# Performance work log

Measured on AMD Instinct MI355X. Metric: run time of the kernel, lower is better.

Reference implementation:

```python
import jax, jax.numpy as jnp
import numpy as np

D_MODEL = 2048
N_HEADS = 32
N_KV = 8
HEAD_DIM = D_MODEL // N_HEADS  # 64
D_FF = 8192
ROPE_BASE = 10000.0
EPS = 1e-5
B, S = 2, 2048


def setup_inputs() -> dict:
    key = jax.random.key(0)
    ks = jax.random.split(key, 8)
    s = 0.02
    qkv_out = (N_HEADS + 2 * N_KV) * HEAD_DIM
    return {
        "x": jax.random.normal(ks[0], (B, S, D_MODEL), jnp.float32),
        "w_norm1": jnp.ones((D_MODEL,), jnp.float32),
        "w_qkv": jax.random.normal(ks[1], (D_MODEL, qkv_out), jnp.float32) * s,
        "w_out": jax.random.normal(ks[2], (D_MODEL, D_MODEL), jnp.float32) * s,
        "w_norm2": jnp.ones((D_MODEL,), jnp.float32),
        "w_gate": jax.random.normal(ks[3], (D_MODEL, D_FF), jnp.float32) * s,
        "w_up": jax.random.normal(ks[4], (D_MODEL, D_FF), jnp.float32) * s,
        "w_down": jax.random.normal(ks[5], (D_FF, D_MODEL), jnp.float32) * s,
    }


def _rmsnorm(x, w):
    var = jnp.mean(x * x, axis=-1, keepdims=True)
    return x * jax.lax.rsqrt(var + EPS) * w


def _rope(x, cos, sin):
    # x: [b, s, h, d]; cos/sin: [s, d/2]; non-interleaved (NeoX half split)
    half = x.shape[-1] // 2
    x1, x2 = x[..., :half], x[..., half:]
    c = cos[None, :, None, :]
    sn = sin[None, :, None, :]
    return jnp.concatenate([x1 * c - x2 * sn, x1 * sn + x2 * c], axis=-1)


def _forward(x, w_norm1, w_qkv, w_out, w_norm2, w_gate, w_up, w_down):
    b, s, d = x.shape
    # --- attention block ---
    h = _rmsnorm(x, w_norm1)
    qkv = h @ w_qkv  # [b, s, (H + 2*KV) * hd]
    q = qkv[..., : N_HEADS * HEAD_DIM].reshape(b, s, N_HEADS, HEAD_DIM)
    kv = qkv[..., N_HEADS * HEAD_DIM:].reshape(b, s, 2, N_KV, HEAD_DIM)
    k, v = kv[:, :, 0], kv[:, :, 1]

    inv_freq = 1.0 / (ROPE_BASE ** (jnp.arange(0, HEAD_DIM, 2, dtype=jnp.float32) / HEAD_DIM))
    t = jnp.arange(s, dtype=jnp.float32)
    freqs = t[:, None] * inv_freq[None, :]  # [s, hd/2]
    cos, sin = jnp.cos(freqs), jnp.sin(freqs)
    q = _rope(q, cos, sin)
    k = _rope(k, cos, sin)

    # GQA: repeat_interleave kv heads to match q heads
    g = N_HEADS // N_KV
    k = jnp.repeat(k, g, axis=2)  # [b, s, H, hd]
    v = jnp.repeat(v, g, axis=2)

    scale = 1.0 / np.sqrt(HEAD_DIM)
    scores = jnp.einsum("bqhd,bkhd->bhqk", q, k) * scale
    causal = jnp.tril(jnp.ones((s, s), bool))
    scores = jnp.where(causal[None, None], scores, jnp.finfo(scores.dtype).min)
    attn = jax.nn.softmax(scores, axis=-1)
    ctx = jnp.einsum("bhqk,bkhd->bqhd", attn, v).reshape(b, s, N_HEADS * HEAD_DIM)
    x = x + ctx @ w_out

    # --- MLP block (SwiGLU) ---
    h2 = _rmsnorm(x, w_norm2)
    mlp = (jax.nn.silu(h2 @ w_gate) * (h2 @ w_up)) @ w_down
    return x + mlp


def reference(x, w_norm1, w_qkv, w_out, w_norm2, w_gate, w_up, w_down):
    return _forward(x, w_norm1, w_qkv, w_out, w_norm2, w_gate, w_up, w_down)
```

## Files before the change

kernel.cpp:

```cpp
#include <hip/hip_runtime.h>
#include <stdint.h>

#define D_MODEL 2048
#define S_LEN   2048
#define NTOK    4096
#define QKV_N   3072
#define DFF     8192

typedef float  f32x4   __attribute__((ext_vector_type(4)));
typedef float  f32x16  __attribute__((ext_vector_type(16)));
typedef __bf16 bf16x8  __attribute__((ext_vector_type(8)));
typedef unsigned short u16;
typedef unsigned short u16x8 __attribute__((ext_vector_type(8)));

__device__ __forceinline__ float b2f(u16 u){ union{float f; uint32_t i;} v; v.i = ((uint32_t)u) << 16; return v.f; }
__device__ __forceinline__ u16 f2b(float f){
  union{float f; uint32_t i;} v; v.f = f;
  uint32_t r = v.i + 0x7FFFu + ((v.i >> 16) & 1u);
  return (u16)(r >> 16);
}

__device__ __forceinline__ void gload_lds16(const void* gsrc, void* ldst){
  __builtin_amdgcn_global_load_lds(
      (const __attribute__((address_space(1))) void*)gsrc,
      (__attribute__((address_space(3))) void*)ldst,
      16, 0, 0);
}

__device__ __forceinline__ void conv_tiles(const float* W, u16* WT,
    int Nfull, int Kt, int Nt, int k0g, int n0g, void* ldsbuf)
{
  if (W == nullptr) return;
  float* tf = (float*)ldsbuf;
  const int tt  = threadIdx.x;
  const int nTn = Nt >> 6;
  const int nT  = (Kt >> 6) * nTn;
  const int bid = blockIdx.y * gridDim.x + blockIdx.x;
  const int gsz = gridDim.x * gridDim.y;
  const int c4 = (tt & 15) << 2;
  const int r  = tt >> 4;
  for (int tile = bid; tile < nT; tile += gsz) {
    const int k0 = (tile / nTn) << 6, n0 = (tile % nTn) << 6;
    __syncthreads();
    if (tt < 256) {
#pragma unroll
      for (int i = 0; i < 4; ++i) {
        int row = r + i * 16;
        float4 v = *reinterpret_cast<const float4*>(&W[(size_t)(k0g + k0 + row) * Nfull + n0g + n0 + c4]);
        tf[row * 65 + c4 + 0] = v.x; tf[row * 65 + c4 + 1] = v.y;
        tf[row * 65 + c4 + 2] = v.z; tf[row * 65 + c4 + 3] = v.w;
      }
    }
    __syncthreads();
    if (tt < 256) {
#pragma unroll
      for (int i = 0; i < 4; ++i) {
        int n = r + i * 16;
        ushort4 ov;
        ov.x = f2b(tf[(c4 + 0) * 65 + n]); ov.y = f2b(tf[(c4 + 1) * 65 + n]);
        ov.z = f2b(tf[(c4 + 2) * 65 + n]); ov.w = f2b(tf[(c4 + 3) * 65 + n]);
        *reinterpret_cast<ushort4*>(&WT[(size_t)(n0 + n) * Kt + k0 + c4]) = ov;
      }
    }
  }
}

__global__ __launch_bounds__(256) void wconv_kernel(const float* __restrict__ W, u16* __restrict__ WT,
                                                    int Nfull, int Kt, int Nt, int k0g, int n0g)
{
  __shared__ float tile[64 * 65];
  conv_tiles(W, WT, Nfull, Kt, Nt, k0g, n0g, tile);
}

__global__ void sincos_kernel(float* __restrict__ ct, float* __restrict__ st)
{
  int idx = blockIdx.x * 256 + threadIdx.x;
  if (idx >= S_LEN * 32) return;
  int p = idx >> 5, i = idx & 31;
  double freq = pow(10000.0, -((double)(2*i)) / 64.0);
  double ang  = (double)p * freq;
  ct[idx] = (float)cos(ang);
  st[idx] = (float)sin(ang);
}

template<bool BF16IN>
__global__ __launch_bounds__(256) void rmsnorm_kernel(const void* __restrict__ xin, const float* __restrict__ w, u16* __restrict__ out,
                                                      const float* cvW, u16* cvWT, int cvNfull, int cvKt, int cvNt, int cvK0g, int cvN0g)
{
  __shared__ float tfbuf[64 * 65];
  const int row = blockIdx.x;
  const int t = threadIdx.x;
  float v[8];
  if (BF16IN) {
    const u16* xr = ((const u16*)xin) + (size_t)row * D_MODEL;
    u16x8 a = *reinterpret_cast<const u16x8*>(&xr[t*8]);
#pragma unroll
    for (int j = 0; j < 8; ++j) v[j] = b2f(a[j]);
  } else {
    const float* xr = ((const float*)xin) + (size_t)row * D_MODEL;
    float4 a = *reinterpret_cast<const float4*>(&xr[t*8]);
    float4 c = *reinterpret_cast<const float4*>(&xr[t*8+4]);
    v[0]=a.x; v[1]=a.y; v[2]=a.z; v[3]=a.w; v[4]=c.x; v[5]=c.y; v[6]=c.z; v[7]=c.w;
  }
  float ss = 0.f;
#pragma unroll
  for (int j = 0; j < 8; ++j) ss += v[j]*v[j];
#pragma unroll
  for (int d = 1; d < 64; d <<= 1) ss += __shfl_xor(ss, d);
  __shared__ float red[4];
  if ((t & 63) == 0) red[t >> 6] = ss;
  __syncthreads();
  ss = red[0] + red[1] + red[2] + red[3];
  const float sc = rsqrtf(ss * (1.0f / (float)D_MODEL) + 1e-5f);
  float4 w0 = *reinterpret_cast<const float4*>(&w[t*8]);
  float4 w1 = *reinterpret_cast<const float4*>(&w[t*8+4]);
  u16x8 o;
  o[0]=f2b(v[0]*sc*w0.x); o[1]=f2b(v[1]*sc*w0.y); o[2]=f2b(v[2]*sc*w0.z); o[3]=f2b(v[3]*sc*w0.w);
  o[4]=f2b(v[4]*sc*w1.x); o[5]=f2b(v[5]*sc*w1.y); o[6]=f2b(v[6]*sc*w1.z); o[7]=f2b(v[7]*sc*w1.w);
  *reinterpret_cast<u16x8*>(&out[(size_t)row * D_MODEL + t*8]) = o;
  conv_tiles(cvW, cvWT, cvNfull, cvKt, cvNt, cvK0g, cvN0g, tfbuf);
}

template<int EPI>
__device__ __forceinline__ void epi_store(size_t idx, float v, float* Cf, u16* Cb,
                                          const float* resf, const u16* resb, const u16* other)
{
  if (EPI == 2)      Cb[idx] = f2b(v / (1.0f + __expf(-v)));
  else if (EPI == 3) Cb[idx] = f2b(v * b2f(other[idx]));
  else if (EPI == 4) Cb[idx] = f2b(v);
  else if (EPI == 5) Cf[idx] += v;
  else if (EPI == 6) Cb[idx] = f2b(v + resf[idx]);
  else if (EPI == 7) Cf[idx] = v + b2f(resb[idx]);
}

template<int EPI>
__global__ __launch_bounds__(512, 2) void gemm8p_kernel(
    const u16* __restrict__ A, const u16* __restrict__ BT,
    int K, int lda, int ldb, int ldc, int n_off,
    float* Cf, u16* Cb,
    const float* __restrict__ resf, const u16* __restrict__ resb, const u16* other,
    const float* cvW, u16* cvWT, int cvNfull, int cvKt, int cvNt, int cvK0g, int cvN0g)
{
  __shared__ u16 lds[65536];
  const int tid = threadIdx.x;
  const int w = tid >> 6, lane = tid & 63;
  const int g = lane >> 4, lr = lane & 15;
  const int wm = w >> 2, wn = w & 3;
  const int bn = blockIdx.x, bm = blockIdx.y;
  const int NT = K >> 6;
  const int NI = NT >> 1;

  const int srow = tid >> 3;
  const int sg   = (tid & 7) ^ (srow & 7);
  const u16* Asrc = A  + (size_t)(bm * 256) * lda;
  const u16* Bsrc = BT + (size_t)(bn * 256) * ldb;

  const int agc0 = ((0 + g) ^ (lr & 7)) * 8;
  const int agc1 = ((4 + g) ^ (lr & 7)) * 8;

  f32x4 acc[8][4];
#pragma unroll
  for (int i = 0; i < 8; ++i)
#pragma unroll
    for (int j = 0; j < 4; ++j) acc[i][j] = (f32x4){0.f, 0.f, 0.f, 0.f};
  bf16x8 af[4][2], bf0[2][2], bf1[2][2];

#define STAGE_H(isB, h, b, T) do {                                           \
    int tc = ((T) < NT) ? (T) : (NT - 1);                                    \
    const u16* sb = (isB) ? Bsrc : Asrc;                                     \
    const int  sld = (isB) ? ldb : lda;                                      \
    const u16* s0 = sb + (size_t)((h)*128 + srow) * sld + tc*64 + sg*8;      \
    u16* dst = &lds[(b)*32768 + (isB)*16384 + (h)*8192 + tid*8];             \
    gload_lds16(s0, dst);                                                    \
    gload_lds16(s0 + (size_t)64 * sld, dst + 4096);                          \
  } while (0)

#define LOADA(mih, b) { _Pragma("unroll") for (int q = 0; q < 4; ++q) {      \
    const u16* rp = &lds[(b)*32768 + (wm*128 + (mih)*64 + q*16 + lr) * 64];  \
    af[q][0] = *(const bf16x8*)(rp + agc0);                                  \
    af[q][1] = *(const bf16x8*)(rp + agc1); } }

#define LOADB(dst, nih, b) { _Pragma("unroll") for (int nq = 0; nq < 2; ++nq) { \
    const u16* rp = &lds[(b)*32768 + 16384 + (wn*64 + (nih)*32 + nq*16 + lr) * 64]; \
    dst[nq][0] = *(const bf16x8*)(rp + agc0);                                \
    dst[nq][1] = *(const bf16x8*)(rp + agc1); } }

#define MM(mih, nih, BF) {                                                   \
    __builtin_amdgcn_s_setprio(1);                                           \
    _Pragma("unroll") for (int kk = 0; kk < 2; ++kk)                         \
      _Pragma("unroll") for (int q = 0; q < 4; ++q)                          \
        _Pragma("unroll") for (int nq = 0; nq < 2; ++nq)                     \
          acc[(mih)*4+q][(nih)*2+nq] = __builtin_amdgcn_mfma_f32_16x16x32_bf16( \
              af[q][kk], BF[nq][kk], acc[(mih)*4+q][(nih)*2+nq], 0, 0, 0);   \
    __builtin_amdgcn_s_setprio(0); }

#define SYNC_MID  __builtin_amdgcn_s_barrier();                              \
                  asm volatile("s_waitcnt lgkmcnt(0)" ::: "memory");         \
                  __builtin_amdgcn_sched_barrier(0);
#define PHEND     __builtin_amdgcn_s_barrier();
#define PHEND_VM  asm volatile("s_waitcnt vmcnt(4)" ::: "memory");           \
                  __builtin_amdgcn_s_barrier();

  STAGE_H(0, 0, 0, 0); STAGE_H(0, 1, 0, 0);
  STAGE_H(1, 0, 0, 0); STAGE_H(1, 1, 0, 0);
  STAGE_H(1, 0, 1, 1); STAGE_H(1, 1, 1, 1);
  asm volatile("s_waitcnt vmcnt(4)" ::: "memory");
  __builtin_amdgcn_s_barrier();

  for (int i = 0; i < NI; ++i) {
    const int t0 = 2 * i;
    LOADA(0, 0); LOADB(bf0, 0, 0);
    STAGE_H(0, 0, 1, t0 + 1);
    SYNC_MID; MM(0, 0, bf0); PHEND;
    LOADB(bf1, 1, 0);
    STAGE_H(0, 1, 1, t0 + 1);
    SYNC_MID; MM(0, 1, bf1); PHEND;
    LOADA(1, 0);
    STAGE_H(1, 0, 0, t0 + 2);
    SYNC_MID; MM(1, 1, bf1); PHEND;
    STAGE_H(1, 1, 0, t0 + 2);
    SYNC_MID; MM(1, 0, bf0); PHEND_VM;
    LOADA(0, 1); LOADB(bf0, 0, 1);
    STAGE_H(0, 0, 0, t0 + 2);
    SYNC_MID; MM(0, 0, bf0); PHEND;
    LOADB(bf1, 1, 1);
    STAGE_H(0, 1, 0, t0 + 2);
    SYNC_MID; MM(0, 1, bf1); PHEND;
    LOADA(1, 1);
    STAGE_H(1, 0, 1, t0 + 3);
    SYNC_MID; MM(1, 1, bf1); PHEND;
    STAGE_H(1, 1, 1, t0 + 3);
    SYNC_MID; MM(1, 0, bf0); PHEND_VM;
  }
#undef STAGE_H
#undef LOADA
#undef LOADB
#undef MM

#pragma unroll
  for (int mi = 0; mi < 8; ++mi) {
    const int rowOff = (mi >> 2) * 64 + (mi & 3) * 16;
#pragma unroll
    for (int ni = 0; ni < 4; ++ni) {
      const int colOff = (ni >> 1) * 32 + (ni & 1) * 16;
#pragma unroll
      for (int j = 0; j < 4; ++j) {
        int row = bm*256 + wm*128 + rowOff + g*4 + j;
        int col = n_off + bn*256 + wn*64 + colOff + lr;
        epi_store<EPI>((size_t)row * ldc + col, acc[mi][ni][j], Cf, Cb, resf, resb, other);
      }
    }
  }
  conv_tiles(cvW, cvWT, cvNfull, cvKt, cvNt, cvK0g, cvN0g, lds);
}

template<int EPI>
__global__ __launch_bounds__(512) void gemm128_kernel(
    const u16* __restrict__ A, const u16* __restrict__ BT,
    int K, int lda, int ldb, int ldc, int n_off,
    float* Cf, u16* Cb,
    const float* __restrict__ resf, const u16* __restrict__ resb, const u16* other,
    const float* cvW, u16* cvWT, int cvNfull, int cvKt, int cvNt, int cvK0g, int cvN0g)
{
  __shared__ u16 lds[49152];
  const int tid = threadIdx.x;
  const int w = tid >> 6, lane = tid & 63;
  const int g = lane >> 4, lr = lane & 15;
  const int wm = w >> 2, wn = w & 3;
  const int bn = blockIdx.x, bm = blockIdx.y;
  const int NT = K >> 6;
  const int NI = NT >> 1;

  const int srow = tid >> 3;
  const int sg   = (tid & 7) ^ (srow & 7);
  const u16* Asrc = A  + (size_t)(bm * 128) * lda;
  const u16* Bsrc = BT + (size_t)(bn * 256) * ldb;

  const int agc0 = ((0 + g) ^ (lr & 7)) * 8;
  const int agc1 = ((4 + g) ^ (lr & 7)) * 8;

  f32x4 acc[4][4];
#pragma unroll
  for (int i = 0; i < 4; ++i)
#pragma unroll
    for (int j = 0; j < 4; ++j) acc[i][j] = (f32x4){0.f, 0.f, 0.f, 0.f};
  bf16x8 af[2][2], bf0[2][2], bf1[2][2];

#define STAGE_A(b, T) do {                                                   \
    int tc = ((T) < NT) ? (T) : (NT - 1);                                    \
    const u16* s0 = Asrc + (size_t)srow * lda + tc*64 + sg*8;                \
    u16* dst = &lds[(b)*24576 + tid*8];                                      \
    gload_lds16(s0, dst);                                                    \
    gload_lds16(s0 + (size_t)64 * lda, dst + 4096);                          \
  } while (0)

#define STAGE_BH(h, b, T) do {                                               \
    int tc = ((T) < NT) ? (T) : (NT - 1);                                    \
    const u16* s0 = Bsrc + (size_t)((h)*128 + srow) * ldb + tc*64 + sg*8;    \
    u16* dst = &lds[(b)*24576 + 8192 + (h)*8192 + tid*8];                    \
    gload_lds16(s0, dst);                                                    \
    gload_lds16(s0 + (size_t)64 * ldb, dst + 4096);                         \
  } while (0)

#define LOADA(mih, b) { _Pragma("unroll") for (int q = 0; q < 2; ++q) {      \
    const u16* rp = &lds[(b)*24576 + (wm*64 + (mih)*32 + q*16 + lr) * 64];   \
    af[q][0] = *(const bf16x8*)(rp + agc0);                                  \
    af[q][1] = *(const bf16x8*)(rp + agc1); } }

#define LOADB(dst, nih, b) { _Pragma("unroll") for (int nq = 0; nq < 2; ++nq) { \
    const u16* rp = &lds[(b)*24576 + 8192 + (wn*64 + (nih)*32 + nq*16 + lr) * 64]; \
    dst[nq][0] = *(const bf16x8*)(rp + agc0);                                \
    dst[nq][1] = *(const bf16x8*)(rp + agc1); } }

#define MM(mih, nih, BF) {                                                   \
    __builtin_amdgcn_s_setprio(1);                                           \
    _Pragma("unroll") for (int kk = 0; kk < 2; ++kk)                         \
      _Pragma("unroll") for (int q = 0; q < 2; ++q)                          \
        _Pragma("unroll") for (int nq = 0; nq < 2; ++nq)                     \
          acc[(mih)*2+q][(nih)*2+nq] = __builtin_amdgcn_mfma_f32_16x16x32_bf16( \
              af[q][kk], BF[nq][kk], acc[(mih)*2+q][(nih)*2+nq], 0, 0, 0);   \
    __builtin_amdgcn_s_setprio(0); }

  STAGE_A(0, 0); STAGE_BH(0, 0, 0); STAGE_BH(1, 0, 0);
  STAGE_BH(0, 1, 1); STAGE_BH(1, 1, 1);
  asm volatile("s_waitcnt vmcnt(4)" ::: "memory");
  __builtin_amdgcn_s_barrier();

  for (int i = 0; i < NI; ++i) {
    const int t0 = 2 * i;
    LOADA(0, 0); LOADB(bf0, 0, 0);
    STAGE_A(1, t0 + 1);
    SYNC_MID; MM(0, 0, bf0); PHEND;
    LOADB(bf1, 1, 0);
    STAGE_BH(0, 0, t0 + 2);
    SYNC_MID; MM(0, 1, bf1); PHEND;
    LOADA(1, 0);
    STAGE_BH(1, 0, t0 + 2);
    SYNC_MID; MM(1, 1, bf1); PHEND;
    STAGE_A(0, t0 + 2);
    SYNC_MID; MM(1, 0, bf0);
    asm volatile("s_waitcnt vmcnt(6)" ::: "memory");
    __builtin_amdgcn_s_barrier();
    LOADA(0, 1); LOADB(bf0, 0, 1);
    SYNC_MID; MM(0, 0, bf0); PHEND;
    LOADB(bf1, 1, 1);
    STAGE_BH(0, 1, t0 + 3);
    SYNC_MID; MM(0, 1, bf1); PHEND;
    LOADA(1, 1);
    STAGE_BH(1, 1, t0 + 3);
    SYNC_MID; MM(1, 1, bf1); PHEND;
    SYNC_MID; MM(1, 0, bf0);
    asm volatile("s_waitcnt vmcnt(4)" ::: "memory");
    __builtin_amdgcn_s_barrier();
  }
#undef STAGE_A
#undef STAGE_BH
#undef LOADA
#undef LOADB
#undef MM
#undef SYNC_MID
#undef PHEND
#undef PHEND_VM

#pragma unroll
  for (int mi = 0; mi < 4; ++mi) {
    const int rowOff = (mi >> 1) * 32 + (mi & 1) * 16;
#pragma unroll
    for (int ni = 0; ni < 4; ++ni) {
      const int colOff = (ni >> 1) * 32 + (ni & 1) * 16;
#pragma unroll
      for (int j = 0; j < 4; ++j) {
        int row = bm*128 + wm*64 + rowOff + g*4 + j;
        int col = n_off + bn*256 + wn*64 + colOff + lr;
        epi_store<EPI>((size_t)row * ldc + col, acc[mi][ni][j], Cf, Cb, resf, resb, other);
      }
    }
  }
  conv_tiles(cvW, cvWT, cvNfull, cvKt, cvNt, cvK0g, cvN0g, lds);
}

__global__ __launch_bounds__(256) void rope_kernel(
    const u16* __restrict__ qkv, const float* __restrict__ ct, const float* __restrict__ st,
    u16* __restrict__ Kt, u16* __restrict__ VT)
{
  const int tok = blockIdx.x;
  const int b = tok >> 11, s = tok & (S_LEN - 1);
  const int w = threadIdx.x >> 6, lane = threadIdx.x & 63;
  const size_t base = (size_t)tok * QKV_N;
  for (int slot = w; slot < 16; slot += 4) {
    int col = (slot < 8) ? 2048 + slot * 64 : 2560 + (slot - 8) * 64;
    float v = b2f(qkv[base + col + lane]);
    if (slot < 8) {
      int i = lane & 31;
      float c = ct[s * 32 + i], sn = st[s * 32 + i];
      float p = b2f(qkv[base + col + (lane ^ 32)]);
      v = (lane < 32) ? (v * c - p * sn) : (v * c + p * sn);
    }
    u16 ob = f2b(v);
    if (slot < 8) Kt[((size_t)(b * 8 + slot)     * S_LEN + s) * 64 + lane] = ob;
    else          VT[((size_t)(b * 8 + slot - 8) * 64 + lane) * S_LEN + s] = ob;
  }
}

#define ASCALE 0.1803368801111204f
__global__ __launch_bounds__(256, 3) void attn_kernel(
    const u16* __restrict__ qkv, const u16* __restrict__ Kt,
    const u16* __restrict__ VT, u16* __restrict__ ctx,
    const float* __restrict__ ct, const float* __restrict__ st,
    const float* cvW, u16* cvWT, int cvNfull, int cvKt, int cvNt, int cvK0g, int cvN0g)
{
  __shared__ float tfbuf[64 * 65];
  const int bh  = blockIdx.x;
  const int qb  = 15 - blockIdx.y;
  const int wid = threadIdx.x >> 6;
  const int lane = threadIdx.x & 63;
  const int b = bh >> 5, h = bh & 31;
  const int kvh = (b << 3) + (h >> 2);
  const int q0 = qb * 128 + wid * 32;
  const int cq = lane & 31;
  const int hi = lane >> 5;

  const u16* Kp = Kt + (size_t)kvh * S_LEN * 64 + cq * 64 + hi * 8;
  const u16* Vbase = VT + (size_t)kvh * 64 * S_LEN + hi * 8;
  const u16* Vp[4];
#pragma unroll
  for (int v = 0; v < 4; ++v)
    Vp[v] = Vbase + (size_t)((v & 1) * 32 + cq) * S_LEN + (v >> 1) * 16;

  bf16x8 qf[4];
  {
    const u16* Qr = qkv + (size_t)(b * S_LEN + q0 + cq) * QKV_N + h * 64 + hi * 8;
    u16 qr[4][8];
#pragma unroll
    for (int t = 0; t < 4; ++t)
      *reinterpret_cast<u16x8*>(qr[t]) = *reinterpret_cast<const u16x8*>(Qr + t * 16);
    const float* cb = ct + (size_t)(q0 + cq) * 32 + hi * 8;
    const float* sb = st + (size_t)(q0 + cq) * 32 + hi * 8;
    union { u16 u[8]; bf16x8 v; } qo[4];
#pragma unroll
    for (int t = 0; t < 2; ++t) {
      float4 c0 = *reinterpret_cast<const float4*>(cb + 16 * t);
      float4 c1 = *reinterpret_cast<const float4*>(cb + 16 * t + 4);
      float4 s0 = *reinterpret_cast<const float4*>(sb + 16 * t);
      float4 s1 = *reinterpret_cast<const float4*>(sb + 16 * t + 4);
      float cc[8] = {c0.x,c0.y,c0.z,c0.w, c1.x,c1.y,c1.z,c1.w};
      float ssn[8] = {s0.x,s0.y,s0.z,s0.w, s1.x,s1.y,s1.z,s1.w};
#pragma unroll
      for (int i = 0; i < 8; ++i) {
        float lo = b2f(qr[t][i]), hif = b2f(qr[t + 2][i]);
        qo[t].u[i]     = f2b(lo * cc[i] - hif * ssn[i]);
        qo[t + 2].u[i] = f2b(hif * cc[i] + lo * ssn[i]);
      }
    }
#pragma unroll
    for (int t = 0; t < 4; ++t) qf[t] = qo[t].v;
  }

  f32x16 o0 = {}, o1 = {};
  float m = -1e30f, l = 0.f;

  __shared__ float xch[4][32];

  const int nt = qb * 4 + wid + 1;

#define ATT_LOADK(KF, T) { _Pragma("unroll") for (int q_ = 0; q_ < 4; ++q_) \
    KF[q_] = *(const bf16x8*)(Kp + (T) * 2048 + q_ * 16); }
#define ATT_LOADV(VF, T) { _Pragma("unroll") for (int v_ = 0; v_ < 4; ++v_) \
    VF[v_] = *(const bf16x8*)(Vp[v_] + (T) * 32); }

#define ATT_COMPUTE(KF, VF, T) do {                                          \
    f32x16 sA = {}, sB = {};                                                 \
    sA = __builtin_amdgcn_mfma_f32_32x32x16_bf16(KF[0], qf[0], sA, 0, 0, 0); \
    sB = __builtin_amdgcn_mfma_f32_32x32x16_bf16(KF[1], qf[1], sB, 0, 0, 0); \
    sA = __builtin_amdgcn_mfma_f32_32x32x16_bf16(KF[2], qf[2], sA, 0, 0, 0); \
    sB = __builtin_amdgcn_mfma_f32_32x32x16_bf16(KF[3], qf[3], sB, 0, 0, 0); \
    float p[16];                                                             \
    _Pragma("unroll") for (int r = 0; r < 16; ++r) p[r] = (sA[r] + sB[r]) * ASCALE; \
    if ((T) == nt - 1) {                                                     \
      _Pragma("unroll") for (int r = 0; r < 16; ++r) {                       \
        int kk = (r & 3) + 8 * (r >> 2) + 4 * hi;                            \
        if (kk > cq) p[r] = -1e30f;                                          \
      }                                                                      \
    }                                                                        \
    float m0_ = fmaxf(fmaxf(p[0], p[1]), p[2]);                              \
    float m1_ = fmaxf(fmaxf(p[3], p[4]), p[5]);                              \
    float m2_ = fmaxf(fmaxf(p[6], p[7]), p[8]);                              \
    float m3_ = fmaxf(fmaxf(p[9], p[10]), p[11]);                            \
    float m4_ = fmaxf(fmaxf(p[12], p[13]), p[14]);                           \
    float tmax = fmaxf(fmaxf(fmaxf(m0_, m1_), m2_), fmaxf(fmaxf(m3_, m4_), p[15])); \
    tmax = fmaxf(tmax, __shfl_xor(tmax, 32));                                \
    if (!__all(tmax <= m + 8.0f)) {                                          \
      float mn = fmaxf(m, tmax);                                             \
      float corr = exp2f(m - mn);                                            \
      m = mn;                                                                \
      l *= corr;                                                             \
      if (hi == 0) xch[wid][cq] = corr;                                      \
      asm volatile("s_waitcnt lgkmcnt(0)" ::: "memory");                     \
      __builtin_amdgcn_sched_barrier(0);                                     \
      float4 c0 = *reinterpret_cast<const float4*>(&xch[wid][4 * hi + 0]);   \
      float4 c1 = *reinterpret_cast<const float4*>(&xch[wid][4 * hi + 8]);   \
      float4 c2 = *reinterpret_cast<const float4*>(&xch[wid][4 * hi + 16]);  \
      float4 c3 = *reinterpret_cast<const float4*>(&xch[wid][4 * hi + 24]);  \
      float ca[16] = {c0.x,c0.y,c0.z,c0.w, c1.x,c1.y,c1.z,c1.w,              \
                      c2.x,c2.y,c2.z,c2.w, c3.x,c3.y,c3.z,c3.w};             \
      _Pragma("unroll") for (int r = 0; r < 16; ++r) { o0[r] *= ca[r]; o1[r] *= ca[r]; } \
    }                                                                        \
    float tsum = 0.f;                                                        \
    _Pragma("unroll") for (int r = 0; r < 16; ++r) { p[r] = exp2f(p[r] - m); tsum += p[r]; } \
    l += tsum;                                                               \
    uint32_t wds[8], pw[8];                                                  \
    _Pragma("unroll") for (int j = 0; j < 8; ++j) {                          \
      uint32_t wv;                                                           \
      asm("v_cvt_pk_bf16_f32 %0, %1, %2" : "=v"(wv) : "v"(p[2*j]), "v"(p[2*j+1])); \
      wds[j] = wv;                                                           \
    }                                                                        \
    _Pragma("unroll") for (int j = 0; j < 8; ++j) pw[j] = __shfl_xor(wds[j], 32); \
    union { uint32_t u[4]; bf16x8 v; } pa0, pa1;                             \
    pa0.u[0] = hi ? pw[2]  : wds[0];                                         \
    pa0.u[1] = hi ? pw[3]  : wds[1];                                         \
    pa0.u[2] = hi ? wds[2] : pw[0];                                          \
    pa0.u[3] = hi ? wds[3] : pw[1];                                          \
    pa1.u[0] = hi ? pw[6]  : wds[4];                                         \
    pa1.u[1] = hi ? pw[7]  : wds[5];                                         \
    pa1.u[2] = hi ? wds[6] : pw[4];                                          \
    pa1.u[3] = hi ? wds[7] : pw[5];                                          \
    o0 = __builtin_amdgcn_mfma_f32_32x32x16_bf16(pa0.v, VF[0], o0, 0, 0, 0); \
    o0 = __builtin_amdgcn_mfma_f32_32x32x16_bf16(pa1.v, VF[2], o0, 0, 0, 0); \
    o1 = __builtin_amdgcn_mfma_f32_32x32x16_bf16(pa0.v, VF[1], o1, 0, 0, 0); \
    o1 = __builtin_amdgcn_mfma_f32_32x32x16_bf16(pa1.v, VF[3], o1, 0, 0, 0); \
  } while (0)

  bf16x8 kf0[4], kf1[4], vf[4];
  ATT_LOADK(kf0, 0);
  for (int t = 0; t < nt; ) {
    if (t + 1 < nt) ATT_LOADK(kf1, t + 1);
    ATT_LOADV(vf, t);
    ATT_COMPUTE(kf0, vf, t);
    ++t; if (t >= nt) break;
    if (t + 1 < nt) ATT_LOADK(kf0, t + 1);
    ATT_LOADV(vf, t);
    ATT_COMPUTE(kf1, vf, t);
    ++t;
  }
#undef ATT_LOADK
#undef ATT_LOADV
#undef ATT_COMPUTE

  l += __shfl_xor(l, 32);
  float linv = 1.0f / l;
  if (hi == 0) xch[wid][cq] = linv;
  asm volatile("s_waitcnt lgkmcnt(0)" ::: "memory");
  __builtin_amdgcn_sched_barrier(0);
  float4 n0 = *reinterpret_cast<const float4*>(&xch[wid][4 * hi + 0]);
  float4 n1 = *reinterpret_cast<const float4*>(&xch[wid][4 * hi + 8]);
  float4 n2 = *reinterpret_cast<const float4*>(&xch[wid][4 * hi + 16]);
  float4 n3 = *reinterpret_cast<const float4*>(&xch[wid][4 * hi + 24]);
  float na[16] = {n0.x,n0.y,n0.z,n0.w, n1.x,n1.y,n1.z,n1.w,
                  n2.x,n2.y,n2.z,n2.w, n3.x,n3.y,n3.z,n3.w};
#pragma unroll
  for (int r = 0; r < 16; ++r) {
    int row = (r & 3) + 8 * (r >> 2) + 4 * hi;
    size_t base = (size_t)(b * S_LEN + q0 + row) * D_MODEL + h * 64;
    ctx[base + cq]      = f2b(o0[r] * na[r]);
    ctx[base + 32 + cq] = f2b(o1[r] * na[r]);
  }
  conv_tiles(cvW, cvWT, cvNfull, cvKt, cvNt, cvK0g, cvN0g, tfbuf);
}

#define NOCV nullptr, nullptr, 0, 0, 0, 0, 0
extern "C" void kernel_launch(void* const* d_in, const int* in_sizes, int n_in,
                              void* d_out, int out_size, void* d_ws, size_t ws_size,
                              hipStream_t stream)
{
  const float* x     = (const float*)d_in[0];
  const float* wn1   = (const float*)d_in[1];
  const float* wqkv  = (const float*)d_in[2];
  const float* wout  = (const float*)d_in[3];
  const float* wn2   = (const float*)d_in[4];
  const float* wgate = (const float*)d_in[5];
  const float* wup   = (const float*)d_in[6];
  const float* wdown = (const float*)d_in[7];
  float* out = (float*)d_out;
  char* ws = (char*)d_ws;

  float* cosT  = (float*)(ws + 0);
  float* sinT  = (float*)(ws + 262144);
  u16*   slotA = (u16*)  (ws + 524288);
  u16*   slotB = (u16*)  (ws + 17301504);
  u16*   x1b   = (u16*)  (ws + 34078720);
  char*  S     = ws + 50855936;
  u16*   hB    = (u16*)(S + 0);
  u16*   qkvB  = (u16*)(S + 16777216);
  u16*   kB    = (u16*)(S + 41943040);
  u16*   vtB   = (u16*)(S + 46137344);
  u16*   ctxB  = (u16*)(S + 0);
  u16*   h2B   = (u16*)(S + 0);
  u16*   slab  = (u16*)(S + 16777216);

  sincos_kernel<<<dim3(256), 256, 0, stream>>>(cosT, sinT);
  rmsnorm_kernel<false><<<dim3(NTOK), 256, 0, stream>>>(x, wn1, hB, NOCV);
  wconv_kernel<<<dim3(1536), 256, 0, stream>>>(wqkv, slotA, 3072, 2048, 3072, 0, 0);

  gemm128_kernel<4><<<dim3(12, 32), 512, 0, stream>>>(hB, slotA, 2048, 2048, 2048, 3072, 0,
      nullptr, qkvB, nullptr, nullptr, nullptr, wout, slotB, 2048, 2048, 2048, 0, 0);
  rope_kernel<<<dim3(NTOK), 256, 0, stream>>>(qkvB, cosT, sinT, kB, vtB);
  attn_kernel<<<dim3(64, 16), 256, 0, stream>>>(qkvB, kB, vtB, ctxB, cosT, sinT,
      wgate, slotA, 8192, 2048, 4096, 0, 0);

  gemm128_kernel<6><<<dim3(8, 32), 512, 0, stream>>>(ctxB, slotB, 2048, 2048, 2048, 2048, 0,
      nullptr, x1b, x, nullptr, nullptr, NOCV);

  rmsnorm_kernel<true><<<dim3(NTOK), 256, 0, stream>>>(x1b, wn2, h2B,
      wup, slotB, 8192, 2048, 4096, 0, 0);

  gemm8p_kernel<2><<<dim3(16, 16), 512, 0, stream>>>(h2B, slotA, 2048, 2048, 2048, 4096, 0,
      nullptr, slab, nullptr, nullptr, nullptr, NOCV);
  gemm8p_kernel<3><<<dim3(16, 16), 512, 0, stream>>>(h2B, slotB, 2048, 2048, 2048, 4096, 0,
      nullptr, slab, nullptr, nullptr, slab, wdown, slotA, 2048, 4096, 2048, 0, 0);
  gemm128_kernel<7><<<dim3(8, 32), 512, 0, stream>>>(slab, slotA, 4096, 4096, 4096, 2048, 0,
      out, nullptr, nullptr, x1b, nullptr, wgate, slotB, 8192, 2048, 4096, 0, 4096);
  gemm8p_kernel<2><<<dim3(16, 16), 512, 0, stream>>>(h2B, slotB, 2048, 2048, 2048, 4096, 0,
      nullptr, slab, nullptr, nullptr, nullptr, wup, slotA, 8192, 2048, 4096, 0, 4096);
  gemm8p_kernel<3><<<dim3(16, 16), 512, 0, stream>>>(h2B, slotA, 2048, 2048, 2048, 4096, 0,
      nullptr, slab, nullptr, nullptr, slab, wdown, slotB, 2048, 4096, 2048, 4096, 0);
  gemm128_kernel<5><<<dim3(8, 32), 512, 0, stream>>>(slab, slotB, 4096, 4096, 4096, 2048, 0,
      out, nullptr, nullptr, nullptr, nullptr, NOCV);
}
```

Measured before the change: 791.4 us.

## Split-K down projection, rebalance causal attention tasks, fold softmax scale into Q

The down-projection GEMMs now use the 256-tile gemm8p kernel with a split-K grid over blockIdx.z. One K half accumulates into the fp32 output and the other writes bf16 partials, which a new add_partials kernel sums at the end. The residual is copied into out by the second rmsnorm. Attention blocks now each process a pair of complementary causal query tiles (jj and 63-jj) to balance work. They also prefetch V alongside K, fold the softmax scale into Q at load time, use a tree sum for l, and lower launch bounds to 2 waves. Storing partials in bf16 loses precision, and the extra partial buffers and reduction pass add memory traffic.

Result: slower. 854.5 us (+8.0%).

```diff
diff --git a/kernel.cpp b/kernel.cpp
--- a/kernel.cpp
+++ b/kernel.cpp
@@ -35,8 +35,8 @@
   const int tt  = threadIdx.x;
   const int nTn = Nt >> 6;
   const int nT  = (Kt >> 6) * nTn;
-  const int bid = blockIdx.y * gridDim.x + blockIdx.x;
-  const int gsz = gridDim.x * gridDim.y;
+  const int bid = (blockIdx.z * gridDim.y + blockIdx.y) * gridDim.x + blockIdx.x;
+  const int gsz = gridDim.x * gridDim.y * gridDim.z;
   const int c4 = (tt & 15) << 2;
   const int r  = tt >> 4;
   for (int tile = bid; tile < nT; tile += gsz) {
@@ -85,6 +85,7 @@
 
 template<bool BF16IN>
 __global__ __launch_bounds__(256) void rmsnorm_kernel(const void* __restrict__ xin, const float* __restrict__ w, u16* __restrict__ out,
+                                                      float* __restrict__ xout,
                                                       const float* cvW, u16* cvWT, int cvNfull, int cvKt, int cvNt, int cvK0g, int cvN0g)
 {
   __shared__ float tfbuf[64 * 65];
@@ -101,6 +102,12 @@
     float4 a = *reinterpret_cast<const float4*>(&xr[t*8]);
     float4 c = *reinterpret_cast<const float4*>(&xr[t*8+4]);
     v[0]=a.x; v[1]=a.y; v[2]=a.z; v[3]=a.w; v[4]=c.x; v[5]=c.y; v[6]=c.z; v[7]=c.w;
+  }
+  if (xout) {
+    float4 o0 = {v[0], v[1], v[2], v[3]};
+    float4 o1 = {v[4], v[5], v[6], v[7]};
+    *reinterpret_cast<float4*>(&xout[(size_t)row * D_MODEL + t*8])     = o0;
+    *reinterpret_cast<float4*>(&xout[(size_t)row * D_MODEL + t*8 + 4]) = o1;
   }
   float ss = 0.f;
 #pragma unroll
@@ -131,12 +138,13 @@
   else if (EPI == 5) Cf[idx] += v;
   else if (EPI == 6) Cb[idx] = f2b(v + resf[idx]);
   else if (EPI == 7) Cf[idx] = v + b2f(resb[idx]);
+  else if (EPI == 8) { if (blockIdx.z == 0) Cf[idx] += v; else Cb[idx] = f2b(v); }
 }
 
 template<int EPI>
 __global__ __launch_bounds__(512, 2) void gemm8p_kernel(
     const u16* __restrict__ A, const u16* __restrict__ BT,
-    int K, int lda, int ldb, int ldc, int n_off,
+    int K, int lda, int ldb, int ldc, int n_off, int kstep,
     float* Cf, u16* Cb,
     const float* __restrict__ resf, const u16* __restrict__ resb, const u16* other,
     const float* cvW, u16* cvWT, int cvNfull, int cvKt, int cvNt, int cvK0g, int cvN0g)
@@ -147,13 +155,14 @@
   const int g = lane >> 4, lr = lane & 15;
   const int wm = w >> 2, wn = w & 3;
   const int bn = blockIdx.x, bm = blockIdx.y;
+  const int koff = blockIdx.z * kstep;
   const int NT = K >> 6;
   const int NI = NT >> 1;
 
   const int srow = tid >> 3;
   const int sg   = (tid & 7) ^ (srow & 7);
-  const u16* Asrc = A  + (size_t)(bm * 256) * lda;
-  const u16* Bsrc = BT + (size_t)(bn * 256) * ldb;
+  const u16* Asrc = A  + (size_t)(bm * 256) * lda + koff;
+  const u16* Bsrc = BT + (size_t)(bn * 256) * ldb + koff;
 
   const int agc0 = ((0 + g) ^ (lr & 7)) * 8;
   const int agc1 = ((4 + g) ^ (lr & 7)) * 8;
@@ -403,7 +412,7 @@
 }
 
 #define ASCALE 0.1803368801111204f
-__global__ __launch_bounds__(256, 3) void attn_kernel(
+__global__ __launch_bounds__(256, 2) void attn_kernel(
     const u16* __restrict__ qkv, const u16* __restrict__ Kt,
     const u16* __restrict__ VT, u16* __restrict__ ctx,
     const float* __restrict__ ct, const float* __restrict__ st,
@@ -411,12 +420,12 @@
 {
   __shared__ float tfbuf[64 * 65];
   const int bh  = blockIdx.x;
-  const int qb  = 15 - blockIdx.y;
+  const int y   = blockIdx.y;
   const int wid = threadIdx.x >> 6;
   const int lane = threadIdx.x & 63;
   const int b = bh >> 5, h = bh & 31;
   const int kvh = (b << 3) + (h >> 2);
-  const int q0 = qb * 128 + wid * 32;
+  const int jj = y * 4 + wid;
   const int cq = lane & 31;
   const int hi = lane >> 5;
 
@@ -427,41 +436,7 @@
   for (int v = 0; v < 4; ++v)
     Vp[v] = Vbase + (size_t)((v & 1) * 32 + cq) * S_LEN + (v >> 1) * 16;
 
-  bf16x8 qf[4];
-  {
-    const u16* Qr = qkv + (size_t)(b * S_LEN + q0 + cq) * QKV_N + h * 64 + hi * 8;
-    u16 qr[4][8];
-#pragma unroll
-    for (int t = 0; t < 4; ++t)
-      *reinterpret_cast<u16x8*>(qr[t]) = *reinterpret_cast<const u16x8*>(Qr + t * 16);
-    const float* cb = ct + (size_t)(q0 + cq) * 32 + hi * 8;
-    const float* sb = st + (size_t)(q0 + cq) * 32 + hi * 8;
-    union { u16 u[8]; bf16x8 v; } qo[4];
-#pragma unroll
-    for (int t = 0; t < 2; ++t) {
-      float4 c0 = *reinterpret_cast<const float4*>(cb + 16 * t);
-      float4 c1 = *reinterpret_cast<const float4*>(cb + 16 * t + 4);
-      float4 s0 = *reinterpret_cast<const float4*>(sb + 16 * t);
-      float4 s1 = *reinterpret_cast<const float4*>(sb + 16 * t + 4);
-      float cc[8] = {c0.x,c0.y,c0.z,c0.w, c1.x,c1.y,c1.z,c1.w};
-      float ssn[8] = {s0.x,s0.y,s0.z,s0.w, s1.x,s1.y,s1.z,s1.w};
-#pragma unroll
-      for (int i = 0; i < 8; ++i) {
-        float lo = b2f(qr[t][i]), hif = b2f(qr[t + 2][i]);
-        qo[t].u[i]     = f2b(lo * cc[i] - hif * ssn[i]);
-        qo[t + 2].u[i] = f2b(hif * cc[i] + lo * ssn[i]);
-      }
-    }
-#pragma unroll
-    for (int t = 0; t < 4; ++t) qf[t] = qo[t].v;
-  }
-
-  f32x16 o0 = {}, o1 = {};
-  float m = -1e30f, l = 0.f;
-
   __shared__ float xch[4][32];
-
-  const int nt = qb * 4 + wid + 1;
 
 #define ATT_LOADK(KF, T) { _Pragma("unroll") for (int q_ = 0; q_ < 4; ++q_) \
     KF[q_] = *(const bf16x8*)(Kp + (T) * 2048 + q_ * 16); }
@@ -475,7 +450,7 @@
     sA = __builtin_amdgcn_mfma_f32_32x32x16_bf16(KF[2], qf[2], sA, 0, 0, 0); \
     sB = __builtin_amdgcn_mfma_f32_32x32x16_bf16(KF[3], qf[3], sB, 0, 0, 0); \
     float p[16];                                                             \
-    _Pragma("unroll") for (int r = 0; r < 16; ++r) p[r] = (sA[r] + sB[r]) * ASCALE; \
+    _Pragma("unroll") for (int r = 0; r < 16; ++r) p[r] = sA[r] + sB[r];     \
     if ((T) == nt - 1) {                                                     \
       _Pragma("unroll") for (int r = 0; r < 16; ++r) {                       \
         int kk = (r & 3) + 8 * (r >> 2) + 4 * hi;                            \
@@ -505,9 +480,13 @@
                       c2.x,c2.y,c2.z,c2.w, c3.x,c3.y,c3.z,c3.w};             \
       _Pragma("unroll") for (int r = 0; r < 16; ++r) { o0[r] *= ca[r]; o1[r] *= ca[r]; } \
     }                                                                        \
-    float tsum = 0.f;                                                        \
-    _Pragma("unroll") for (int r = 0; r < 16; ++r) { p[r] = exp2f(p[r] - m); tsum += p[r]; } \
-    l += tsum;                                                               \
+    _Pragma("unroll") for (int r = 0; r < 16; ++r) p[r] = exp2f(p[r] - m);   \
+    {                                                                        \
+      float a0 = p[0]+p[1], a1 = p[2]+p[3], a2 = p[4]+p[5], a3 = p[6]+p[7];  \
+      float a4 = p[8]+p[9], a5 = p[10]+p[11], a6 = p[12]+p[13], a7 = p[14]+p[15]; \
+      float b0_ = a0+a1, b1_ = a2+a3, b2_ = a4+a5, b3_ = a6+a7;              \
+      l += (b0_+b1_) + (b2_+b3_);                                            \
+    }                                                                        \
     uint32_t wds[8], pw[8];                                                  \
     _Pragma("unroll") for (int j = 0; j < 8; ++j) {                          \
       uint32_t wv;                                                           \
@@ -530,41 +509,95 @@
     o1 = __builtin_amdgcn_mfma_f32_32x32x16_bf16(pa1.v, VF[3], o1, 0, 0, 0); \
   } while (0)
 
-  bf16x8 kf0[4], kf1[4], vf[4];
-  ATT_LOADK(kf0, 0);
-  for (int t = 0; t < nt; ) {
-    if (t + 1 < nt) ATT_LOADK(kf1, t + 1);
-    ATT_LOADV(vf, t);
-    ATT_COMPUTE(kf0, vf, t);
-    ++t; if (t >= nt) break;
-    if (t + 1 < nt) ATT_LOADK(kf0, t + 1);
-    ATT_LOADV(vf, t);
-    ATT_COMPUTE(kf1, vf, t);
-    ++t;
+#pragma unroll 1
+  for (int task = 0; task < 2; ++task) {
+    const int qt = task ? (63 - jj) : jj;
+    const int q0 = qt << 5;
+    const int nt = qt + 1;
+
+    bf16x8 qf[4];
+    {
+      const u16* Qr = qkv + (size_t)(b * S_LEN + q0 + cq) * QKV_N + h * 64 + hi * 8;
+      u16 qr[4][8];
+#pragma unroll
+      for (int t = 0; t < 4; ++t)
+        *reinterpret_cast<u16x8*>(qr[t]) = *reinterpret_cast<const u16x8*>(Qr + t * 16);
+      const float* cb = ct + (size_t)(q0 + cq) * 32 + hi * 8;
+      const float* sb = st + (size_t)(q0 + cq) * 32 + hi * 8;
+      union { u16 u[8]; bf16x8 v; } qo[4];
+#pragma unroll
+      for (int t = 0; t < 2; ++t) {
+        float4 c0 = *reinterpret_cast<const float4*>(cb + 16 * t);
+        float4 c1 = *reinterpret_cast<const float4*>(cb + 16 * t + 4);
+        float4 s0 = *reinterpret_cast<const float4*>(sb + 16 * t);
+        float4 s1 = *reinterpret_cast<const float4*>(sb + 16 * t + 4);
+        float cc[8] = {c0.x,c0.y,c0.z,c0.w, c1.x,c1.y,c1.z,c1.w};
+        float ssn[8] = {s0.x,s0.y,s0.z,s0.w, s1.x,s1.y,s1.z,s1.w};
+#pragma unroll
+        for (int i = 0; i < 8; ++i) {
+          float lo = b2f(qr[t][i]), hif = b2f(qr[t + 2][i]);
+          qo[t].u[i]     = f2b((lo * cc[i] - hif * ssn[i]) * ASCALE);
+          qo[t + 2].u[i] = f2b((hif * cc[i] + lo * ssn[i]) * ASCALE);
+        }
+      }
+#pragma unroll
+      for (int t = 0; t < 4; ++t) qf[t] = qo[t].v;
+    }
+
+    f32x16 o0 = {}, o1 = {};
+    float m = -1e30f, l = 0.f;
+
+    bf16x8 kf0[4], kf1[4], vf0[4], vf1[4];
+    ATT_LOADK(kf0, 0); ATT_LOADV(vf0, 0);
+    for (int t = 0; t < nt; ) {
+      if (t + 1 < nt) { ATT_LOADK(kf1, t + 1); ATT_LOADV(vf1, t + 1); }
+      ATT_COMPUTE(kf0, vf0, t);
+      ++t; if (t >= nt) break;
+      if (t + 1 < nt) { ATT_LOADK(kf0, t + 1); ATT_LOADV(vf0, t + 1); }
+      ATT_COMPUTE(kf1, vf1, t);
+      ++t;
+    }
+
+    l += __shfl_xor(l, 32);
+    float linv = 1.0f / l;
+    if (hi == 0) xch[wid][cq] = linv;
+    asm volatile("s_waitcnt lgkmcnt(0)" ::: "memory");
+    __builtin_amdgcn_sched_barrier(0);
+    float4 n0 = *reinterpret_cast<const float4*>(&xch[wid][4 * hi + 0]);
+    float4 n1 = *reinterpret_cast<const float4*>(&xch[wid][4 * hi + 8]);
+    float4 n2 = *reinterpret_cast<const float4*>(&xch[wid][4 * hi + 16]);
+    float4 n3 = *reinterpret_cast<const float4*>(&xch[wid][4 * hi + 24]);
+    float na[16] = {n0.x,n0.y,n0.z,n0.w, n1.x,n1.y,n1.z,n1.w,
+                    n2.x,n2.y,n2.z,n2.w, n3.x,n3.y,n3.z,n3.w};
+#pragma unroll
+    for (int r = 0; r < 16; ++r) {
+      int row = (r & 3) + 8 * (r >> 2) + 4 * hi;
+      size_t base = (size_t)(b * S_LEN + q0 + row) * D_MODEL + h * 64;
+      ctx[base + cq]      = f2b(o0[r] * na[r]);
+      ctx[base + 32 + cq] = f2b(o1[r] * na[r]);
+    }
   }
 #undef ATT_LOADK
 #undef ATT_LOADV
 #undef ATT_COMPUTE
 
-  l += __shfl_xor(l, 32);
-  float linv = 1.0f / l;
-  if (hi == 0) xch[wid][cq] = linv;
-  asm volatile("s_waitcnt lgkmcnt(0)" ::: "memory");
-  __builtin_amdgcn_sched_barrier(0);
-  float4 n0 = *reinterpret_cast<const float4*>(&xch[wid][4 * hi + 0]);
-  float4 n1 = *reinterpret_cast<const float4*>(&xch[wid][4 * hi + 8]);
-  float4 n2 = *reinterpret_cast<const float4*>(&xch[wid][4 * hi + 16]);
-  float4 n3 = *reinterpret_cast<const float4*>(&xch[wid][4 * hi + 24]);
-  float na[16] = {n0.x,n0.y,n0.z,n0.w, n1.x,n1.y,n1.z,n1.w,
-                  n2.x,n2.y,n2.z,n2.w, n3.x,n3.y,n3.z,n3.w};
-#pragma unroll
-  for (int r = 0; r < 16; ++r) {
-    int row = (r & 3) + 8 * (r >> 2) + 4 * hi;
-    size_t base = (size_t)(b * S_LEN + q0 + row) * D_MODEL + h * 64;
-    ctx[base + cq]      = f2b(o0[r] * na[r]);
-    ctx[base + 32 + cq] = f2b(o1[r] * na[r]);
-  }
   conv_tiles(cvW, cvWT, cvNfull, cvKt, cvNt, cvK0g, cvN0g, tfbuf);
+}
+
+__global__ __launch_bounds__(256) void add_partials(float* __restrict__ out,
+    const u16* __restrict__ tA, const u16* __restrict__ tB)
+{
+  size_t i = ((size_t)blockIdx.x * 256 + threadIdx.x) * 8;
+  u16x8 a = *reinterpret_cast<const u16x8*>(tA + i);
+  u16x8 c = *reinterpret_cast<const u16x8*>(tB + i);
+  float4 o0 = *reinterpret_cast<const float4*>(out + i);
+  float4 o1 = *reinterpret_cast<const float4*>(out + i + 4);
+  o0.x += b2f(a[0]) + b2f(c[0]); o0.y += b2f(a[1]) + b2f(c[1]);
+  o0.z += b2f(a[2]) + b2f(c[2]); o0.w += b2f(a[3]) + b2f(c[3]);
+  o1.x += b2f(a[4]) + b2f(c[4]); o1.y += b2f(a[5]) + b2f(c[5]);
+  o1.z += b2f(a[6]) + b2f(c[6]); o1.w += b2f(a[7]) + b2f(c[7]);
+  *reinterpret_cast<float4*>(out + i)     = o0;
+  *reinterpret_cast<float4*>(out + i + 4) = o1;
 }
 
 #define NOCV nullptr, nullptr, 0, 0, 0, 0, 0
@@ -596,33 +629,36 @@
   u16*   ctxB  = (u16*)(S + 0);
   u16*   h2B   = (u16*)(S + 0);
   u16*   slab  = (u16*)(S + 16777216);
+  u16*   tmpA  = x1b;
+  u16*   tmpB  = (u16*)(ws + 101187584);
 
   sincos_kernel<<<dim3(256), 256, 0, stream>>>(cosT, sinT);
-  rmsnorm_kernel<false><<<dim3(NTOK), 256, 0, stream>>>(x, wn1, hB, NOCV);
+  rmsnorm_kernel<false><<<dim3(NTOK), 256, 0, stream>>>(x, wn1, hB, nullptr, NOCV);
   wconv_kernel<<<dim3(1536), 256, 0, stream>>>(wqkv, slotA, 3072, 2048, 3072, 0, 0);
 
   gemm128_kernel<4><<<dim3(12, 32), 512, 0, stream>>>(hB, slotA, 2048, 2048, 2048, 3072, 0,
       nullptr, qkvB, nullptr, nullptr, nullptr, wout, slotB, 2048, 2048, 2048, 0, 0);
   rope_kernel<<<dim3(NTOK), 256, 0, stream>>>(qkvB, cosT, sinT, kB, vtB);
-  attn_kernel<<<dim3(64, 16), 256, 0, stream>>>(qkvB, kB, vtB, ctxB, cosT, sinT,
+  attn_kernel<<<dim3(64, 8), 256, 0, stream>>>(qkvB, kB, vtB, ctxB, cosT, sinT,
       wgate, slotA, 8192, 2048, 4096, 0, 0);
 
   gemm128_kernel<6><<<dim3(8, 32), 512, 0, stream>>>(ctxB, slotB, 2048, 2048, 2048, 2048, 0,
       nullptr, x1b, x, nullptr, nullptr, NOCV);
 
-  rmsnorm_kernel<true><<<dim3(NTOK), 256, 0, stream>>>(x1b, wn2, h2B,
+  rmsnorm_kernel<true><<<dim3(NTOK), 256, 0, stream>>>(x1b, wn2, h2B, out,
       wup, slotB, 8192, 2048, 4096, 0, 0);
 
-  gemm8p_kernel<2><<<dim3(16, 16), 512, 0, stream>>>(h2B, slotA, 2048, 2048, 2048, 4096, 0,
+  gemm8p_kernel<2><<<dim3(16, 16), 512, 0, stream>>>(h2B, slotA, 2048, 2048, 2048, 4096, 0, 0,
       nullptr, slab, nullptr, nullptr, nullptr, NOCV);
-  gemm8p_kernel<3><<<dim3(16, 16), 512, 0, stream>>>(h2B, slotB, 2048, 2048, 2048, 4096, 0,
+  gemm8p_kernel<3><<<dim3(16, 16), 512, 0, stream>>>(h2B, slotB, 2048, 2048, 2048, 4096, 0, 0,
       nullptr, slab, nullptr, nullptr, slab, wdown, slotA, 2048, 4096, 2048, 0, 0);
-  gemm128_kernel<7><<<dim3(8, 32), 512, 0, stream>>>(slab, slotA, 4096, 4096, 4096, 2048, 0,
-      out, nullptr, nullptr, x1b, nullptr, wgate, slotB, 8192, 2048, 4096, 0, 4096);
-  gemm8p_kernel<2><<<dim3(16, 16), 512, 0, stream>>>(h2B, slotB, 2048, 2048, 2048, 4096, 0,
+  gemm8p_kernel<8><<<dim3(8, 16, 2), 512, 0, stream>>>(slab, slotA, 2048, 4096, 4096, 2048, 0, 2048,
+      out, tmpA, nullptr, nullptr, nullptr, wgate, slotB, 8192, 2048, 4096, 0, 4096);
+  gemm8p_kernel<2><<<dim3(16, 16), 512, 0, stream>>>(h2B, slotB, 2048, 2048, 2048, 4096, 0, 0,
       nullptr, slab, nullptr, nullptr, nullptr, wup, slotA, 8192, 2048, 4096, 0, 4096);
-  gemm8p_kernel<3><<<dim3(16, 16), 512, 0, stream>>>(h2B, slotA, 2048, 2048, 2048, 4096, 0,
+  gemm8p_kernel<3><<<dim3(16, 16), 512, 0, stream>>>(h2B, slotA, 2048, 2048, 2048, 4096, 0, 0,
       nullptr, slab, nullptr, nullptr, slab, wdown, slotB, 2048, 4096, 2048, 4096, 0);
-  gemm128_kernel<5><<<dim3(8, 32), 512, 0, stream>>>(slab, slotB, 4096, 4096, 4096, 2048, 0,
-      out, nullptr, nullptr, nullptr, nullptr, NOCV);
-}
+  gemm8p_kernel<8><<<dim3(8, 16, 2), 512, 0, stream>>>(slab, slotB, 2048, 4096, 4096, 2048, 0, 2048,
+      out, tmpB, nullptr, nullptr, nullptr, NOCV);
+  add_partials<<<dim3(4096), 256, 0, stream>>>(out, tmpA, tmpB);
+}
```
